# Kernel optimization log

Hardware: AMD Instinct MI355X
Metric: run time of the kernel (lower is better)

## Reference

```python
import jax, jax.numpy as jnp
import numpy as np

ETA = 1e-5  # option['eta']


def setup_inputs() -> dict:
    key = jax.random.key(0)
    k1, k2, k3, k4 = jax.random.split(key, 4)
    d, N, two_m = 1024, 20000, 512  # num_feature, num_data, 2*m
    At = jax.random.normal(k1, (d, N), dtype=jnp.float32)
    b = jax.random.normal(k2, (N,), dtype=jnp.float32)
    w1_init = jax.random.normal(k3, (d,), dtype=jnp.float32)
    W2_init = jax.random.normal(k4, (two_m, d - 1), dtype=jnp.float32)
    return {"At": At, "b": b, "w1_init": w1_init, "W2_init": W2_init}


def _ftrl_scan(At, b, w1_init, W2_init):
    # Sequential FTRL-style online FM update (task='reg'), faithful to the torch loop.
    def step(carry, xs):
        w1, W2, g_w1, g_W2 = carry
        x, bi = xs                     # x: (d,), bi: scalar
        a = x[:-1]                     # alpha[:-1], (d-1,)
        t = W2 @ a                     # (2m,) == W2.matmul(alpha[:-1])
        scalar = jnp.dot(w1, x) + jnp.dot(t, t)   # w1^T x + t^T t
        sign = 2.0 * (scalar - bi)     # grad of squared loss
        g_w1 = g_w1 + sign * x
        g_W2 = g_W2 + 2.0 * jnp.outer(t, a)       # 2 * (W2 a) a^T
        w1_new = -ETA * g_w1
        W2_new = -ETA * g_W2
        return (w1_new, W2_new, g_w1, g_W2), scalar

    carry0 = (w1_init, W2_init, jnp.zeros_like(w1_init), jnp.zeros_like(W2_init))
    _, preds = jax.lax.scan(step, carry0, (At.T, b))  # scan over num_data
    return preds


def reference(At, b, w1_init, W2_init):
    preds = _ftrl_scan(At, b, w1_init, W2_init)
    return preds, b  # (pred_list, real_list)
```

## Files before the change

### kernel.cpp

```cpp
#include <hip/hip_runtime.h>


#define NN 20000
#define CC 40
#define NCH 500
#define ETA2 2e-5f

#define OFF_GRAM 0L
#define OFF_ZR   390016L
#define OFF_Z1   902016L
#define OFF_S1   1414016L
#define OFF_S2   1926016L
#define OFF_SCLP 2438016L
#define OFF_ACC  2438056L
#define OFF_TV   2458056L

__device__ __forceinline__ void async16(const float* g, float* l) {
  __builtin_amdgcn_global_load_lds(
      (const __attribute__((address_space(1))) void*)g,
      (__attribute__((address_space(3))) void*)l, 16, 0, 0);
}

__global__ __launch_bounds__(1024) void k_init(
    const float* __restrict__ At, const float* __restrict__ bvec,
    const float* __restrict__ w1, const float* __restrict__ W2,
    float* __restrict__ out, float* __restrict__ scalp) {
  __shared__ float x0s[1024];
  __shared__ float part[16];
  const int bid = blockIdx.x, t = threadIdx.x;
  const int wid = t >> 6, lane = t & 63;

  if (bid < 32) {
    x0s[t] = (t < 1023) ? At[(long)t * NN] : 0.f;
    __syncthreads();
    const int row = bid * 16 + wid;
    float p = 0.f;
#pragma unroll
    for (int k = 0; k < 16; ++k) {
      const int ci = k * 64 + lane;
      if (ci < 1023) p = fmaf(W2[(long)row * 1023 + ci], x0s[ci], p);
    }
#pragma unroll
    for (int o = 32; o > 0; o >>= 1) p += __shfl_down(p, o);
    if (lane == 0) part[wid] = p * p;
    __syncthreads();
    if (t == 0) {
      float s = 0.f;
#pragma unroll
      for (int k = 0; k < 16; ++k) s += part[k];
      scalp[bid] = s;
    }
  } else if (bid == 32) {
    float p = w1[t] * At[(long)t * NN];
#pragma unroll
    for (int o = 32; o > 0; o >>= 1) p += __shfl_down(p, o);
    if (lane == 0) part[wid] = p;
    __syncthreads();
    if (t == 0) {
      float s = 0.f;
#pragma unroll
      for (int k = 0; k < 16; ++k) s += part[k];
      scalp[32] = s;
    }
  } else {
    const int i = (bid - 33) * 1000 + t;
    if (t < 1000) out[NN + i] = bvec[i];
  }
}

struct GramSh {
  __align__(16) float xt[2][5120];
  float scr[2640];
  float x0s[1024];
  float up[160];
  __align__(16) float rs[CC];
  float sc[2];
};
static_assert(sizeof(GramSh) <= 64 * 1024, "LDS overflow");

__global__ __launch_bounds__(1024, 8) void k_gram(
    const float* __restrict__ At, const float* __restrict__ bvec,
    float* __restrict__ gram, float* __restrict__ Zr,
    const float* __restrict__ scalp, float* __restrict__ acc) {
  __shared__ GramSh sh;
  const int c = blockIdx.x, t = threadIdx.x;
  const long i0 = (long)c * CC;

  sh.x0s[t] = At[(long)t * NN];
  if (t == 0) {
    float T = 0.f;
#pragma unroll
    for (int k = 0; k < 32; ++k) T += scalp[k];
    sh.sc[0] = T;
    sh.sc[1] = scalp[32];
  }

  const float* g1 = At + (long)(t / 10) * NN + i0 + 4 * (t % 10);
  const float* g2 =
      At + (long)((1024 + t) / 10) * NN + i0 + 4 * ((1024 + t) % 10);

  const bool act = (t < 220);
  int a = 0, bb = 0, band = 0, tile = 0;
  if (act) {
    tile = t % 55; band = t / 55;
    int r = tile; while (r > a) { r -= ++a; } bb = r;
  }
  const bool uact = (t >= 220 && t < 380);
  const int uz = t - 220;
  const int uband = uz / 40, ui = uz - uband * 40;
  float uacc = 0.f;

  float ac[4][4];
#pragma unroll
  for (int r = 0; r < 4; ++r)
#pragma unroll
    for (int s = 0; s < 4; ++s) ac[r][s] = 0.f;

  async16(g1, &sh.xt[0][4 * t]);
  if (t < 256) async16(g2, &sh.xt[0][4096 + 4 * t]);
  __syncthreads();

  const int e0g = band * 32;
  const int e0u = uband * 32;

  for (int st = 0; st < 8; ++st) {
    const float* __restrict__ xs = sh.xt[st & 1];
    if (st < 7) {
      const long adv = (long)(st + 1) * (128L * NN);
      float* nb = sh.xt[(st + 1) & 1];
      async16(g1 + adv, &nb[4 * t]);
      if (t < 256) async16(g2 + adv, &nb[4096 + 4 * t]);
    }
    if (act) {
#pragma unroll 4
      for (int le = e0g; le < e0g + 32; ++le) {
        const float* row = xs + le * 40;
        const float4 ra = *(const float4*)(row + 4 * a);
        const float4 rb = *(const float4*)(row + 4 * bb);
        ac[0][0] = fmaf(ra.x, rb.x, ac[0][0]); ac[0][1] = fmaf(ra.x, rb.y, ac[0][1]);
        ac[0][2] = fmaf(ra.x, rb.z, ac[0][2]); ac[0][3] = fmaf(ra.x, rb.w, ac[0][3]);
        ac[1][0] = fmaf(ra.y, rb.x, ac[1][0]); ac[1][1] = fmaf(ra.y, rb.y, ac[1][1]);
        ac[1][2] = fmaf(ra.y, rb.z, ac[1][2]); ac[1][3] = fmaf(ra.y, rb.w, ac[1][3]);
        ac[2][0] = fmaf(ra.z, rb.x, ac[2][0]); ac[2][1] = fmaf(ra.z, rb.y, ac[2][1]);
        ac[2][2] = fmaf(ra.z, rb.z, ac[2][2]); ac[2][3] = fmaf(ra.z, rb.w, ac[2][3]);
        ac[3][0] = fmaf(ra.w, rb.x, ac[3][0]); ac[3][1] = fmaf(ra.w, rb.y, ac[3][1]);
        ac[3][2] = fmaf(ra.w, rb.z, ac[3][2]); ac[3][3] = fmaf(ra.w, rb.w, ac[3][3]);
      }
    } else if (uact) {
#pragma unroll 4
      for (int le = e0u; le < e0u + 32; ++le)
        uacc = fmaf(xs[le * 40 + ui], sh.x0s[st * 128 + le], uacc);
    }
    __syncthreads();
  }
  if (uact) sh.up[uz] = uacc;
  __syncthreads();

  if (t < CC) {
    const long gi = i0 + t;
    const float uu = sh.up[t] + sh.up[40 + t] + sh.up[80 + t] + sh.up[120 + t];
    const float qi = sh.xt[1][127 * 40 + t];
    const float q0 = sh.x0s[1023];
    const float al = (gi == 0) ? 1.f : -ETA2 * (uu - q0 * qi);
    const float T0 = sh.sc[0], s0v = sh.sc[1];
    const float bv = bvec[gi];
    float r = 2.f * fmaf(al * al, T0, -bv);
    if (gi == 0) r = 2.f * (s0v + T0 - bv);
    sh.rs[t] = r;
    acc[gi] = r;
  }
  if (act && band > 0) {
#pragma unroll
    for (int r = 0; r < 4; ++r)
#pragma unroll
      for (int s = 0; s < 4; ++s)
        sh.scr[(band - 1) * 880 + tile * 16 + r * 4 + s] = ac[r][s];
  }
  __syncthreads();

  {
    const float* xr = At + (long)t * NN + i0;
    float z = 0.f;
#pragma unroll
    for (int j4 = 0; j4 < 10; ++j4) {
      const float4 x = *(const float4*)(xr + 4 * j4);
      const float4 rq = *(const float4*)&sh.rs[4 * j4];
      z = fmaf(x.x, rq.x, z); z = fmaf(x.y, rq.y, z);
      z = fmaf(x.z, rq.z, z); z = fmaf(x.w, rq.w, z);
    }
    Zr[(long)c * 1024 + t] = z;
  }

  if (act && band == 0) {
    float* gp = gram + (long)c * 780;
#pragma unroll
    for (int r = 0; r < 4; ++r) {
      const int row = 4 * a + r;
      const int base = row * (row - 1) / 2;
#pragma unroll
      for (int s = 0; s < 4; ++s) {
        const int col = 4 * bb + s;
        if (col < row)
          gp[base + col] = ac[r][s] + sh.scr[tile * 16 + r * 4 + s] +
                           sh.scr[880 + tile * 16 + r * 4 + s] +
                           sh.scr[1760 + tile * 16 + r * 4 + s];
      }
    }
  }
}

__global__ __launch_bounds__(1024) void k_scan(const float* __restrict__ Z,
                                               float* __restrict__ S) {
  __shared__ float gsum[16][64];
  const int t = threadIdx.x;
  const int ei = t & 63, ci = t >> 6;
  const int e = blockIdx.x * 64 + ei;
  const int c0 = ci * 32;
  const int c1 = (c0 + 32 < NCH) ? c0 + 32 : NCH;

  float s = 0.f;
  for (int base = c0; base < c1; base += 8) {
    float v[8];
#pragma unroll
    for (int k = 0; k < 8; ++k) {
      const int c = base + k;
      v[k] = (c < c1) ? Z[(long)c * 1024 + e] : 0.f;
    }
#pragma unroll
    for (int k = 0; k < 8; ++k) s += v[k];
  }
  gsum[ci][ei] = s;
  __syncthreads();

  float off = 0.f;
  for (int k = 0; k < ci; ++k) off += gsum[k][ei];

  s = off;
  for (int base = c0; base < c1; base += 8) {
    float v[8];
#pragma unroll
    for (int k = 0; k < 8; ++k) {
      const int c = base + k;
      v[k] = (c < c1) ? Z[(long)c * 1024 + e] : 0.f;
    }
#pragma unroll
    for (int k = 0; k < 8; ++k) {
      const int c = base + k;
      if (c < c1) S[(long)c * 1024 + e] = s;
      s += v[k];
    }
  }
}

template <bool LAST>
__global__ __launch_bounds__(1024, 8) void k_term(
    const float* __restrict__ At, const float* __restrict__ bvec,
    const float* __restrict__ gram, const float* __restrict__ S,
    float* __restrict__ Z1, float* __restrict__ acc, float* __restrict__ tvec,
    float* __restrict__ out) {
  __shared__ float Sm[1024];
  __shared__ float red[1024];
  __shared__ __align__(16) float vvs[CC], wvs[CC];
  const int c = blockIdx.x, t = threadIdx.x;
  const long i0 = (long)c * CC;

  Sm[t] = S[(long)c * 1024 + t];
  if (t < CC) vvs[t] = LAST ? tvec[i0 + t] : acc[i0 + t];
  __syncthreads();

  {
    const int ti = t & 63, te = t >> 6;
    float p = 0.f;
    if (ti < CC) {
      const float* col = At + i0 + ti;
      const int e0 = te * 64;
#pragma unroll 8
      for (int e = e0; e < e0 + 64; ++e) p = fmaf(col[(long)e * NN], Sm[e], p);
    }
    red[t] = p;
  }
  __syncthreads();

  if (t < CC) {
    const int i = t;
    float dot = 0.f;
#pragma unroll
    for (int k = 0; k < 16; ++k) dot += red[k * 64 + i];
    const float* grow = gram + (long)c * 780 + i * (i - 1) / 2;
    float g = 0.f;
#pragma unroll 4
    for (int j = 0; j < i; ++j) g = fmaf(grow[j], vvs[j], g);
    const float w = -ETA2 * (dot + g);
    if (LAST) {
      out[i0 + i] = fmaf(0.5f, acc[i0 + i] + w, bvec[i0 + i]);
    } else {
      wvs[i] = w;
      tvec[i0 + i] = w;
      acc[i0 + i] += w;
    }
  }
  if (!LAST) {
    __syncthreads();
    const float* xr = At + (long)t * NN + i0;
    float z = 0.f;
#pragma unroll
    for (int j4 = 0; j4 < 10; ++j4) {
      const float4 x = *(const float4*)(xr + 4 * j4);
      const float4 wq = *(const float4*)&wvs[4 * j4];
      z = fmaf(x.x, wq.x, z); z = fmaf(x.y, wq.y, z);
      z = fmaf(x.z, wq.z, z); z = fmaf(x.w, wq.w, z);
    }
    Z1[(long)c * 1024 + t] = z;
  }
}

extern "C" void kernel_launch(void* const* d_in, const int* in_sizes, int n_in,
                              void* d_out, int out_size, void* d_ws,
                              size_t ws_size, hipStream_t stream) {
  const float* At = (const float*)d_in[0];
  const float* b  = (const float*)d_in[1];
  const float* w1 = (const float*)d_in[2];
  const float* W2 = (const float*)d_in[3];
  float* out = (float*)d_out;
  float* ws = (float*)d_ws;

  float* gram  = ws + OFF_GRAM;
  float* Zr    = ws + OFF_ZR;
  float* Z1    = ws + OFF_Z1;
  float* S1    = ws + OFF_S1;
  float* S2    = ws + OFF_S2;
  float* scalp = ws + OFF_SCLP;
  float* acc   = ws + OFF_ACC;
  float* tvec  = ws + OFF_TV;

  k_init<<<dim3(53), dim3(1024), 0, stream>>>(At, b, w1, W2, out, scalp);
  k_gram<<<dim3(NCH), dim3(1024), 0, stream>>>(At, b, gram, Zr, scalp, acc);
  k_scan<<<dim3(16), dim3(1024), 0, stream>>>(Zr, S1);
  k_term<false><<<dim3(NCH), dim3(1024), 0, stream>>>(At, b, gram, S1, Z1, acc,
                                                      tvec, out);
  k_scan<<<dim3(16), dim3(1024), 0, stream>>>(Z1, S2);
  k_term<true><<<dim3(NCH), dim3(1024), 0, stream>>>(At, b, gram, S2, Z1, acc,
                                                     tvec, out);
}
```

Baseline: 228.8 us.

## Register-staged prefetch in gram, cached x0 column, wider scan grid, more unrolling

The gram kernel stops using async global-to-LDS loads. It now prefetches the next stage into registers and writes them to LDS behind a single inline waitcnt+barrier per stage, dropping the trailing __syncthreads. The strided x0 column is gathered once in k_init into workspace, and k_gram reads it contiguously instead of doing 1024 strided loads per block. The u-dot threads switch to float4 accumulation with fewer threads, k_scan uses 32 blocks with shorter chunks, and several unroll factors are raised. The one-barrier scheme depends on the double buffer and the waitcnt being ordered correctly, and the register prefetch adds register pressure.

```diff
diff --git a/kernel.cpp b/kernel.cpp
--- a/kernel.cpp
+++ b/kernel.cpp
@@ -14,17 +14,13 @@
 #define OFF_SCLP 2438016L
 #define OFF_ACC  2438056L
 #define OFF_TV   2458056L
-
-__device__ __forceinline__ void async16(const float* g, float* l) {
-  __builtin_amdgcn_global_load_lds(
-      (const __attribute__((address_space(1))) void*)g,
-      (__attribute__((address_space(3))) void*)l, 16, 0, 0);
-}
+#define OFF_X0   2478080L
 
 __global__ __launch_bounds__(1024) void k_init(
     const float* __restrict__ At, const float* __restrict__ bvec,
     const float* __restrict__ w1, const float* __restrict__ W2,
-    float* __restrict__ out, float* __restrict__ scalp) {
+    float* __restrict__ out, float* __restrict__ scalp,
+    float* __restrict__ x0ws) {
   __shared__ float x0s[1024];
   __shared__ float part[16];
   const int bid = blockIdx.x, t = threadIdx.x;
@@ -51,7 +47,9 @@
       scalp[bid] = s;
     }
   } else if (bid == 32) {
-    float p = w1[t] * At[(long)t * NN];
+    const float xv = At[(long)t * NN];
+    x0ws[t] = xv;
+    float p = w1[t] * xv;
 #pragma unroll
     for (int o = 32; o > 0; o >>= 1) p += __shfl_down(p, o);
     if (lane == 0) part[wid] = p;
@@ -80,13 +78,14 @@
 
 __global__ __launch_bounds__(1024, 8) void k_gram(
     const float* __restrict__ At, const float* __restrict__ bvec,
-    float* __restrict__ gram, float* __restrict__ Zr,
-    const float* __restrict__ scalp, float* __restrict__ acc) {
+    const float* __restrict__ x0g, float* __restrict__ gram,
+    float* __restrict__ Zr, const float* __restrict__ scalp,
+    float* __restrict__ acc) {
   __shared__ GramSh sh;
   const int c = blockIdx.x, t = threadIdx.x;
   const long i0 = (long)c * CC;
 
-  sh.x0s[t] = At[(long)t * NN];
+  sh.x0s[t] = x0g[t];
   if (t == 0) {
     float T = 0.f;
 #pragma unroll
@@ -105,10 +104,10 @@
     tile = t % 55; band = t / 55;
     int r = tile; while (r > a) { r -= ++a; } bb = r;
   }
-  const bool uact = (t >= 220 && t < 380);
+  const bool uact = (t >= 220 && t < 260);
   const int uz = t - 220;
-  const int uband = uz / 40, ui = uz - uband * 40;
-  float uacc = 0.f;
+  const int uband = uz / 10, uq = uz - uband * 10;
+  float4 uac4 = make_float4(0.f, 0.f, 0.f, 0.f);
 
   float ac[4][4];
 #pragma unroll
@@ -116,21 +115,24 @@
 #pragma unroll
     for (int s = 0; s < 4; ++s) ac[r][s] = 0.f;
 
-  async16(g1, &sh.xt[0][4 * t]);
-  if (t < 256) async16(g2, &sh.xt[0][4096 + 4 * t]);
-  __syncthreads();
+  float4 r1 = *(const float4*)g1;
+  float4 r2 = make_float4(0.f, 0.f, 0.f, 0.f);
+  if (t < 256) r2 = *(const float4*)g2;
 
   const int e0g = band * 32;
   const int e0u = uband * 32;
 
   for (int st = 0; st < 8; ++st) {
-    const float* __restrict__ xs = sh.xt[st & 1];
+    float* nb = sh.xt[st & 1];
+    *(float4*)&nb[4 * t] = r1;
+    if (t < 256) *(float4*)&nb[4096 + 4 * t] = r2;
     if (st < 7) {
       const long adv = (long)(st + 1) * (128L * NN);
-      float* nb = sh.xt[(st + 1) & 1];
-      async16(g1 + adv, &nb[4 * t]);
-      if (t < 256) async16(g2 + adv, &nb[4096 + 4 * t]);
-    }
+      r1 = *(const float4*)(g1 + adv);
+      if (t < 256) r2 = *(const float4*)(g2 + adv);
+    }
+    asm volatile("s_waitcnt lgkmcnt(0)\n\ts_barrier" ::: "memory");
+    const float* __restrict__ xs = sh.xt[st & 1];
     if (act) {
 #pragma unroll 4
       for (int le = e0g; le < e0g + 32; ++le) {
@@ -148,12 +150,17 @@
       }
     } else if (uact) {
 #pragma unroll 4
-      for (int le = e0u; le < e0u + 32; ++le)
-        uacc = fmaf(xs[le * 40 + ui], sh.x0s[st * 128 + le], uacc);
-    }
-    __syncthreads();
-  }
-  if (uact) sh.up[uz] = uacc;
+      for (int le = e0u; le < e0u + 32; ++le) {
+        const float4 v = *(const float4*)(xs + le * 40 + 4 * uq);
+        const float xv = sh.x0s[st * 128 + le];
+        uac4.x = fmaf(xv, v.x, uac4.x);
+        uac4.y = fmaf(xv, v.y, uac4.y);
+        uac4.z = fmaf(xv, v.z, uac4.z);
+        uac4.w = fmaf(xv, v.w, uac4.w);
+      }
+    }
+  }
+  if (uact) *(float4*)&sh.up[uband * 40 + 4 * uq] = uac4;
   __syncthreads();
 
   if (t < CC) {
@@ -211,20 +218,20 @@
 
 __global__ __launch_bounds__(1024) void k_scan(const float* __restrict__ Z,
                                                float* __restrict__ S) {
-  __shared__ float gsum[16][64];
+  __shared__ float gsum[32][32];
   const int t = threadIdx.x;
-  const int ei = t & 63, ci = t >> 6;
-  const int e = blockIdx.x * 64 + ei;
-  const int c0 = ci * 32;
-  const int c1 = (c0 + 32 < NCH) ? c0 + 32 : NCH;
+  const int ei = t & 31, ci = t >> 5;
+  const int e = blockIdx.x * 32 + ei;
+  const int c0 = ci * 16;
+  const int c1 = (c0 + 16 < NCH) ? c0 + 16 : NCH;
 
   float s = 0.f;
   for (int base = c0; base < c1; base += 8) {
     float v[8];
 #pragma unroll
     for (int k = 0; k < 8; ++k) {
-      const int c = base + k;
-      v[k] = (c < c1) ? Z[(long)c * 1024 + e] : 0.f;
+      const int cc = base + k;
+      v[k] = (cc < c1) ? Z[(long)cc * 1024 + e] : 0.f;
     }
 #pragma unroll
     for (int k = 0; k < 8; ++k) s += v[k];
@@ -233,20 +240,22 @@
   __syncthreads();
 
   float off = 0.f;
-  for (int k = 0; k < ci; ++k) off += gsum[k][ei];
+#pragma unroll
+  for (int k = 0; k < 31; ++k)
+    if (k < ci) off += gsum[k][ei];
 
   s = off;
   for (int base = c0; base < c1; base += 8) {
     float v[8];
 #pragma unroll
     for (int k = 0; k < 8; ++k) {
-      const int c = base + k;
-      v[k] = (c < c1) ? Z[(long)c * 1024 + e] : 0.f;
+      const int cc = base + k;
+      v[k] = (cc < c1) ? Z[(long)cc * 1024 + e] : 0.f;
     }
 #pragma unroll
     for (int k = 0; k < 8; ++k) {
-      const int c = base + k;
-      if (c < c1) S[(long)c * 1024 + e] = s;
+      const int cc = base + k;
+      if (cc < c1) S[(long)cc * 1024 + e] = s;
       s += v[k];
     }
   }
@@ -274,7 +283,7 @@
     if (ti < CC) {
       const float* col = At + i0 + ti;
       const int e0 = te * 64;
-#pragma unroll 8
+#pragma unroll 16
       for (int e = e0; e < e0 + 64; ++e) p = fmaf(col[(long)e * NN], Sm[e], p);
     }
     red[t] = p;
@@ -288,7 +297,7 @@
     for (int k = 0; k < 16; ++k) dot += red[k * 64 + i];
     const float* grow = gram + (long)c * 780 + i * (i - 1) / 2;
     float g = 0.f;
-#pragma unroll 4
+#pragma unroll 8
     for (int j = 0; j < i; ++j) g = fmaf(grow[j], vvs[j], g);
     const float w = -ETA2 * (dot + g);
     if (LAST) {
@@ -332,13 +341,15 @@
   float* scalp = ws + OFF_SCLP;
   float* acc   = ws + OFF_ACC;
   float* tvec  = ws + OFF_TV;
-
-  k_init<<<dim3(53), dim3(1024), 0, stream>>>(At, b, w1, W2, out, scalp);
-  k_gram<<<dim3(NCH), dim3(1024), 0, stream>>>(At, b, gram, Zr, scalp, acc);
-  k_scan<<<dim3(16), dim3(1024), 0, stream>>>(Zr, S1);
+  float* x0ws  = ws + OFF_X0;
+
+  k_init<<<dim3(53), dim3(1024), 0, stream>>>(At, b, w1, W2, out, scalp, x0ws);
+  k_gram<<<dim3(NCH), dim3(1024), 0, stream>>>(At, b, x0ws, gram, Zr, scalp,
+                                               acc);
+  k_scan<<<dim3(32), dim3(1024), 0, stream>>>(Zr, S1);
   k_term<false><<<dim3(NCH), dim3(1024), 0, stream>>>(At, b, gram, S1, Z1, acc,
                                                       tvec, out);
-  k_scan<<<dim3(16), dim3(1024), 0, stream>>>(Z1, S2);
+  k_scan<<<dim3(32), dim3(1024), 0, stream>>>(Z1, S2);
   k_term<true><<<dim3(NCH), dim3(1024), 0, stream>>>(At, b, gram, S2, Z1, acc,
                                                      tvec, out);
 }
```

Result: no change. 225.7 us (-1.3%).
